# Optimization experiments

Measured on AMD Instinct MI355X. Metric: run time of the kernel, lower is better.

## Reference

```python
import jax, jax.numpy as jnp
import numpy as np

N_HEAD = 8
D_HEAD = 16
D_MODEL = 128
LEN_Q = 256
MEM_LEN = 256
BATCH = 4


def setup_inputs() -> dict:
    key = jax.random.key(0)
    k1, k2, k3, k4, k5 = jax.random.split(key, 5)
    h = jax.random.normal(k1, (LEN_Q, BATCH, D_MODEL), dtype=jnp.float32)
    mems = jax.random.normal(k2, (MEM_LEN, BATCH, D_MODEL), dtype=jnp.float32)
    # nn.Linear weights are [out_features, in_features]
    Wq = jax.random.normal(k3, (N_HEAD * D_HEAD, D_MODEL), dtype=jnp.float32) / np.sqrt(D_MODEL)
    Wk = jax.random.normal(k4, (N_HEAD * D_HEAD, D_MODEL), dtype=jnp.float32) / np.sqrt(D_MODEL)
    paramR = jax.random.normal(k5, (N_HEAD,), dtype=jnp.float32)
    return {"h": h, "mems": mems, "Wq": Wq, "Wk": Wk, "paramR": paramR}


def reference(h, mems, Wq, Wk, paramR):
    # h: [Lq, B, Dm], mems: [M, B, Dm]
    c = jnp.concatenate([mems, h], axis=0)  # [Lk, B, Dm]
    Lq, B = h.shape[0], h.shape[1]
    Lk = c.shape[0]
    # Linear (no bias): x @ W.T, then split heads and move to [H, B, L, Dh]
    head_q = (h @ Wq.T).reshape(Lq, B, N_HEAD, D_HEAD).transpose(2, 1, 0, 3)
    head_k = (c @ Wk.T).reshape(Lk, B, N_HEAD, D_HEAD).transpose(2, 1, 0, 3)
    # Pairwise difference: [H, B, Lq, Lk, Dh]
    diff = head_q[:, :, :, None, :] - head_k[:, :, None, :, :]
    scaled = diff * paramR[:, None, None, None, None] / jnp.pi
    # torch.sinc == jnp.sinc (normalized sinc, sinc(0)=1)
    score = jnp.abs(jnp.prod(jnp.sinc(scaled), axis=4))  # [H, B, Lq, Lk]
    # permute(2, 3, 1, 0) -> [Lq, Lk, B, H]
    return score.transpose(2, 3, 1, 0)
```

## Files before the change

kernel.cpp:

```cpp
#include <hip/hip_runtime.h>
#include <math.h>

#define LQ 256
#define MEML 256
#define LK 512
#define BB 4
#define NH 8
#define DM 128

#define IT 8
#define QSTRIDE 20

constexpr float INV2PI = 0.15915494309189535f;

__global__ __launch_bounds__(128) void proj_kernel(
    const float* __restrict__ hh, const float* __restrict__ mems,
    const float* __restrict__ Wq, const float* __restrict__ Wk,
    const float* __restrict__ paramR,
    float* __restrict__ qs, float* __restrict__ ksT)
{
    __shared__ float x[8 * 128];
    const int blk = blockIdx.x;
    const int t = threadIdx.x;
    const bool isQ = (blk < 128);
    const int row0 = isQ ? blk * 8 : (blk - 128) * 8;
    const float* __restrict__ W = isQ ? Wq : Wk;

    for (int r = 0; r < 8; ++r) {
        const int row = row0 + r;
        const float* src = isQ ? (hh + row * DM)
                               : ((row < MEML * BB) ? (mems + row * DM)
                                                    : (hh + (row - MEML * BB) * DM));
        x[r * 128 + t] = src[t];
    }
    __syncthreads();

    float acc[8] = {0, 0, 0, 0, 0, 0, 0, 0};
    const float* wrow = W + t * DM;
    for (int k = 0; k < DM; k += 4) {
        const float4 w = *(const float4*)(wrow + k);
        #pragma unroll
        for (int r = 0; r < 8; ++r) {
            acc[r] += x[r * 128 + k + 0] * w.x + x[r * 128 + k + 1] * w.y
                    + x[r * 128 + k + 2] * w.z + x[r * 128 + k + 3] * w.w;
        }
    }
    const int h = t >> 4, d = t & 15;
    const float rs = paramR[h] * INV2PI;
    if (isQ) {
        float* dst = qs + row0 * 128 + t;
        #pragma unroll
        for (int r = 0; r < 8; ++r) dst[r * 128] = acc[r] * rs;
    } else {
        #pragma unroll
        for (int r = 0; r < 8; ++r) {
            const int row = row0 + r;
            const int j = row >> 2, b = row & 3;
            ksT[((d >> 2) * LK + j) * 128 + (b * 8 + h) * 4 + (d & 3)] = acc[r] * rs;
        }
    }
}

__global__ __launch_bounds__(256, 8) void score_kernel(
    const float* __restrict__ qs, const float* __restrict__ ksT,
    float* __restrict__ out)
{
    __shared__ float qt[IT * 32 * QSTRIDE];
    const int t = threadIdx.x;
    const int bh = t & 31;
    const int js = t >> 5;
    const int key = bh >> 3;
    const int i0 = blockIdx.x * IT;
    const int j = blockIdx.y * 8 + js;

    constexpr float i2 = INV2PI * INV2PI;
    constexpr float i4 = i2 * i2;
    constexpr float i8 = i4 * i4;
    constexpr float C16 = i8 * i8;
    constexpr float EPS = 2.0e-4f * INV2PI;

    {
        const float* src = qs + i0 * 32 * 16;
        #pragma unroll
        for (int rep = 0; rep < 4; ++rep) {
            const int c4 = rep * 256 + t;
            const int row = c4 >> 2, cc = (c4 & 3) * 4;
            const float4 v = *(const float4*)(src + c4 * 4);
            *(float4*)(&qt[row * QSTRIDE + cc]) = v;
        }
    }

    float k[16];
    #pragma unroll
    for (int s = 0; s < 4; ++s) {
        const int plane = s ^ key;
        const float4 v = *(const float4*)(ksT + (plane * LK + j) * 128 + bh * 4);
        k[s * 4 + 0] = v.x; k[s * 4 + 1] = v.y;
        k[s * 4 + 2] = v.z; k[s * 4 + 3] = v.w;
    }
    __syncthreads();

    #pragma unroll 4
    for (int ii = 0; ii < IT; ++ii) {
        const float* qrow = &qt[(ii * 32 + bh) * QSTRIDE];
        float q[16];
        #pragma unroll
        for (int s = 0; s < 4; ++s) {
            const float4 v = *(const float4*)(qrow + ((s ^ key) << 2));
            q[s * 4 + 0] = v.x; q[s * 4 + 1] = v.y;
            q[s * 4 + 2] = v.z; q[s * 4 + 3] = v.w;
        }
        float pn0 = 1.f, pd0 = 1.f, pn1 = 1.f, pd1 = 1.f;
        #pragma unroll
        for (int d = 0; d < 16; ++d) {
            const float u2 = fmaxf(__builtin_fabsf(q[d] - k[d]), EPS);
            const float s = __builtin_amdgcn_sinf(u2);
            if (d < 8) { pn0 *= s; pd0 *= u2; }
            else       { pn1 *= s; pd1 *= u2; }
        }
        const float r0 = pn0 * __builtin_amdgcn_rcpf(pd0);
        const float r1 = pn1 * __builtin_amdgcn_rcpf(pd1);
        out[((i0 + ii) * LK + j) * 32 + bh] = __builtin_fabsf(r0 * r1) * C16;
    }
}

extern "C" void kernel_launch(void* const* d_in, const int* in_sizes, int n_in,
                              void* d_out, int out_size, void* d_ws, size_t ws_size,
                              hipStream_t stream) {
    const float* hh     = (const float*)d_in[0];
    const float* mems   = (const float*)d_in[1];
    const float* Wq     = (const float*)d_in[2];
    const float* Wk     = (const float*)d_in[3];
    const float* paramR = (const float*)d_in[4];
    float* out = (float*)d_out;

    float* qs  = (float*)d_ws;
    float* ksT = qs + LQ * BB * DM;

    proj_kernel<<<384, 128, 0, stream>>>(hh, mems, Wq, Wk, paramR, qs, ksT);
    score_kernel<<<dim3(LQ / IT, LK / 8), 256, 0, stream>>>(qs, ksT, out);
}
```

Baseline: 29.81 us.

## Store Q in planar layout and read it directly, dropping shared-memory staging

The projection kernel now writes Q in the same plane-major layout as K, so the score kernel loads each Q row with coalesced float4 global reads. This removes the LDS staging, the XOR swizzle and the block barrier. The rows per block are halved, which doubles the grid. The cost is that every warp (8 per block, one per j) re-reads Q from global/L2 instead of sharing one LDS copy, which adds redundant memory traffic.

```diff
diff --git a/kernel.cpp b/kernel.cpp
--- a/kernel.cpp
+++ b/kernel.cpp
@@ -8,8 +8,7 @@
 #define NH 8
 #define DM 128
 
-#define IT 8
-#define QSTRIDE 20
+#define IT 4
 
 constexpr float INV2PI = 0.15915494309189535f;
 
@@ -17,7 +16,7 @@
     const float* __restrict__ hh, const float* __restrict__ mems,
     const float* __restrict__ Wq, const float* __restrict__ Wk,
     const float* __restrict__ paramR,
-    float* __restrict__ qs, float* __restrict__ ksT)
+    float* __restrict__ qsP, float* __restrict__ ksT)
 {
     __shared__ float x[8 * 128];
     const int blk = blockIdx.x;
@@ -47,29 +46,28 @@
     }
     const int h = t >> 4, d = t & 15;
     const float rs = paramR[h] * INV2PI;
-    if (isQ) {
-        float* dst = qs + row0 * 128 + t;
-        #pragma unroll
-        for (int r = 0; r < 8; ++r) dst[r * 128] = acc[r] * rs;
-    } else {
-        #pragma unroll
-        for (int r = 0; r < 8; ++r) {
-            const int row = row0 + r;
-            const int j = row >> 2, b = row & 3;
-            ksT[((d >> 2) * LK + j) * 128 + (b * 8 + h) * 4 + (d & 3)] = acc[r] * rs;
+    #pragma unroll
+    for (int r = 0; r < 8; ++r) {
+        const int row = row0 + r;
+        const int b = row & 3;
+        const float v = acc[r] * rs;
+        if (isQ) {
+            const int i = row >> 2;
+            qsP[((d >> 2) * LQ + i) * 128 + (b * 8 + h) * 4 + (d & 3)] = v;
+        } else {
+            const int j = row >> 2;
+            ksT[((d >> 2) * LK + j) * 128 + (b * 8 + h) * 4 + (d & 3)] = v;
         }
     }
 }
 
 __global__ __launch_bounds__(256, 8) void score_kernel(
-    const float* __restrict__ qs, const float* __restrict__ ksT,
+    const float* __restrict__ qsP, const float* __restrict__ ksT,
     float* __restrict__ out)
 {
-    __shared__ float qt[IT * 32 * QSTRIDE];
     const int t = threadIdx.x;
     const int bh = t & 31;
     const int js = t >> 5;
-    const int key = bh >> 3;
     const int i0 = blockIdx.x * IT;
     const int j = blockIdx.y * 8 + js;
 
@@ -79,48 +77,37 @@
     constexpr float C16 = i8 * i8;
     constexpr float EPS = 2.0e-4f * INV2PI;
 
-    {
-        const float* src = qs + i0 * 32 * 16;
-        #pragma unroll
-        for (int rep = 0; rep < 4; ++rep) {
-            const int c4 = rep * 256 + t;
-            const int row = c4 >> 2, cc = (c4 & 3) * 4;
-            const float4 v = *(const float4*)(src + c4 * 4);
-            *(float4*)(&qt[row * QSTRIDE + cc]) = v;
-        }
-    }
-
     float k[16];
     #pragma unroll
     for (int s = 0; s < 4; ++s) {
-        const int plane = s ^ key;
-        const float4 v = *(const float4*)(ksT + (plane * LK + j) * 128 + bh * 4);
+        const float4 v = *(const float4*)(ksT + (s * LK + j) * 128 + bh * 4);
         k[s * 4 + 0] = v.x; k[s * 4 + 1] = v.y;
         k[s * 4 + 2] = v.z; k[s * 4 + 3] = v.w;
     }
-    __syncthreads();
 
-    #pragma unroll 4
+    #pragma unroll 2
     for (int ii = 0; ii < IT; ++ii) {
-        const float* qrow = &qt[(ii * 32 + bh) * QSTRIDE];
-        float q[16];
+        const int i = i0 + ii;
+        float4 qv[4];
+        #pragma unroll
+        for (int s = 0; s < 4; ++s)
+            qv[s] = *(const float4*)(qsP + (s * LQ + i) * 128 + bh * 4);
+
+        float pn0 = 1.f, pd0 = 1.f, pn1 = 1.f, pd1 = 1.f;
         #pragma unroll
         for (int s = 0; s < 4; ++s) {
-            const float4 v = *(const float4*)(qrow + ((s ^ key) << 2));
-            q[s * 4 + 0] = v.x; q[s * 4 + 1] = v.y;
-            q[s * 4 + 2] = v.z; q[s * 4 + 3] = v.w;
-        }
-        float pn0 = 1.f, pd0 = 1.f, pn1 = 1.f, pd1 = 1.f;
-        #pragma unroll
-        for (int d = 0; d < 16; ++d) {
-            const float u2 = fmaxf(__builtin_fabsf(q[d] - k[d]), EPS);
-            const float s = __builtin_amdgcn_sinf(u2);
-            if (d < 8) { pn0 *= s; pd0 *= u2; }
-            else       { pn1 *= s; pd1 *= u2; }
+            const float qq[4] = {qv[s].x, qv[s].y, qv[s].z, qv[s].w};
+            #pragma unroll
+            for (int dd = 0; dd < 4; ++dd) {
+                const float u2 = fmaxf(__builtin_fabsf(qq[dd] - k[s * 4 + dd]), EPS);
+                const float sn = __builtin_amdgcn_sinf(u2);
+                if (s < 2) { pn0 *= sn; pd0 *= u2; }
+                else       { pn1 *= sn; pd1 *= u2; }
+            }
         }
         const float r0 = pn0 * __builtin_amdgcn_rcpf(pd0);
         const float r1 = pn1 * __builtin_amdgcn_rcpf(pd1);
-        out[((i0 + ii) * LK + j) * 32 + bh] = __builtin_fabsf(r0 * r1) * C16;
+        out[(i * LK + j) * 32 + bh] = __builtin_fabsf(r0 * r1) * C16;
     }
 }
 
@@ -134,9 +121,9 @@
     const float* paramR = (const float*)d_in[4];
     float* out = (float*)d_out;
 
-    float* qs  = (float*)d_ws;
-    float* ksT = qs + LQ * BB * DM;
+    float* qsP = (float*)d_ws;
+    float* ksT = qsP + LQ * BB * DM;
 
-    proj_kernel<<<384, 128, 0, stream>>>(hh, mems, Wq, Wk, paramR, qs, ksT);
-    score_kernel<<<dim3(LQ / IT, LK / 8), 256, 0, stream>>>(qs, ksT, out);
+    proj_kernel<<<384, 128, 0, stream>>>(hh, mems, Wq, Wk, paramR, qsP, ksT);
+    score_kernel<<<dim3(LQ / IT, LK / 8), 256, 0, stream>>>(qsP, ksT, out);
 }
```

Measured after the change: 34.28 us. 1.15x slower.

## Replace hardware sine with packed polynomial sine over paired head dimensions

Applied to the files above, without the earlier changes.

Swaps the per-element v_sin transcendental for a range-reduced odd polynomial evaluated on two-wide float vectors, so the compiler can emit packed FP32 FMA/mul instructions. The projection output layout is permuted so that dimensions d and d+8 sit next to each other, which lets the two partial products be packed. Occupancy hint is lowered from 8 to 4 waves and the unroll is reduced to make room for the extra registers. The polynomial costs more ALU ops than one transcendental and relies on the rounding-based range reduction being accurate enough.

```diff
diff --git a/kernel.cpp b/kernel.cpp
--- a/kernel.cpp
+++ b/kernel.cpp
@@ -12,6 +12,16 @@
 #define QSTRIDE 20
 
 constexpr float INV2PI = 0.15915494309189535f;
+
+typedef float v2f __attribute__((ext_vector_type(2)));
+
+#define SC1   6.2831853071795865f
+#define SC3  -41.341702240399755f
+#define SC5   81.60524927607504f
+#define SC7  -76.70585975306136f
+#define SC9   42.05869394489765f
+#define SC11 -15.094642576059076f
+#define SC13  3.8199525848482824f
 
 __global__ __launch_bounds__(128) void proj_kernel(
     const float* __restrict__ hh, const float* __restrict__ mems,
@@ -46,9 +56,10 @@
         }
     }
     const int h = t >> 4, d = t & 15;
+    const int e = ((d & 7) << 1) | (d >> 3);
     const float rs = paramR[h] * INV2PI;
     if (isQ) {
-        float* dst = qs + row0 * 128 + t;
+        float* dst = qs + row0 * 128 + h * 16 + e;
         #pragma unroll
         for (int r = 0; r < 8; ++r) dst[r * 128] = acc[r] * rs;
     } else {
@@ -56,12 +67,12 @@
         for (int r = 0; r < 8; ++r) {
             const int row = row0 + r;
             const int j = row >> 2, b = row & 3;
-            ksT[((d >> 2) * LK + j) * 128 + (b * 8 + h) * 4 + (d & 3)] = acc[r] * rs;
+            ksT[((e >> 2) * LK + j) * 128 + (b * 8 + h) * 4 + (e & 3)] = acc[r] * rs;
         }
     }
 }
 
-__global__ __launch_bounds__(256, 8) void score_kernel(
+__global__ __launch_bounds__(256, 4) void score_kernel(
     const float* __restrict__ qs, const float* __restrict__ ksT,
     float* __restrict__ out)
 {
@@ -73,10 +84,10 @@
     const int i0 = blockIdx.x * IT;
     const int j = blockIdx.y * 8 + js;
 
-    constexpr float i2 = INV2PI * INV2PI;
-    constexpr float i4 = i2 * i2;
-    constexpr float i8 = i4 * i4;
-    constexpr float C16 = i8 * i8;
+    constexpr float i2c = INV2PI * INV2PI;
+    constexpr float i4c = i2c * i2c;
+    constexpr float i8c = i4c * i4c;
+    constexpr float C16 = i8c * i8c;
     constexpr float EPS = 2.0e-4f * INV2PI;
 
     {
@@ -90,36 +101,54 @@
         }
     }
 
-    float k[16];
+    v2f kp[8];
     #pragma unroll
     for (int s = 0; s < 4; ++s) {
         const int plane = s ^ key;
         const float4 v = *(const float4*)(ksT + (plane * LK + j) * 128 + bh * 4);
-        k[s * 4 + 0] = v.x; k[s * 4 + 1] = v.y;
-        k[s * 4 + 2] = v.z; k[s * 4 + 3] = v.w;
+        kp[s * 2 + 0] = v2f{v.x, v.y};
+        kp[s * 2 + 1] = v2f{v.z, v.w};
     }
     __syncthreads();
 
-    #pragma unroll 4
+    #pragma unroll 2
     for (int ii = 0; ii < IT; ++ii) {
         const float* qrow = &qt[(ii * 32 + bh) * QSTRIDE];
-        float q[16];
+        v2f qp[8];
         #pragma unroll
         for (int s = 0; s < 4; ++s) {
             const float4 v = *(const float4*)(qrow + ((s ^ key) << 2));
-            q[s * 4 + 0] = v.x; q[s * 4 + 1] = v.y;
-            q[s * 4 + 2] = v.z; q[s * 4 + 3] = v.w;
+            qp[s * 2 + 0] = v2f{v.x, v.y};
+            qp[s * 2 + 1] = v2f{v.z, v.w};
         }
-        float pn0 = 1.f, pd0 = 1.f, pn1 = 1.f, pd1 = 1.f;
+        v2f pnA = v2f{1.f, 1.f}, pdA = v2f{1.f, 1.f};
+        v2f pnB = v2f{1.f, 1.f}, pdB = v2f{1.f, 1.f};
         #pragma unroll
-        for (int d = 0; d < 16; ++d) {
-            const float u2 = fmaxf(__builtin_fabsf(q[d] - k[d]), EPS);
-            const float s = __builtin_amdgcn_sinf(u2);
-            if (d < 8) { pn0 *= s; pd0 *= u2; }
-            else       { pn1 *= s; pd1 *= u2; }
+        for (int p = 0; p < 8; ++p) {
+            const v2f u = qp[p] - kp[p];
+            v2f a;
+            a.x = fmaxf(__builtin_fabsf(u.x), EPS);
+            a.y = fmaxf(__builtin_fabsf(u.y), EPS);
+            v2f n;
+            n.x = __builtin_rintf(a.x);
+            n.y = __builtin_rintf(a.y);
+            const v2f f  = a - n;
+            const v2f f2 = f * f;
+            v2f pl = v2f{SC13, SC13};
+            pl = pl * f2 + v2f{SC11, SC11};
+            pl = pl * f2 + v2f{SC9,  SC9};
+            pl = pl * f2 + v2f{SC7,  SC7};
+            pl = pl * f2 + v2f{SC5,  SC5};
+            pl = pl * f2 + v2f{SC3,  SC3};
+            pl = pl * f2 + v2f{SC1,  SC1};
+            const v2f s = f * pl;
+            if (p < 4) { pnA *= s; pdA *= a; }
+            else       { pnB *= s; pdB *= a; }
         }
-        const float r0 = pn0 * __builtin_amdgcn_rcpf(pd0);
-        const float r1 = pn1 * __builtin_amdgcn_rcpf(pd1);
+        const float n0 = pnA.x * pnB.x, d0 = pdA.x * pdB.x;
+        const float n1 = pnA.y * pnB.y, d1 = pdA.y * pdB.y;
+        const float r0 = n0 * __builtin_amdgcn_rcpf(d0);
+        const float r1 = n1 * __builtin_amdgcn_rcpf(d1);
         out[((i0 + ii) * LK + j) * 32 + bh] = __builtin_fabsf(r0 * r1) * C16;
     }
 }
```

After: 37.14 us. +24.6%, slower.
